# Kernel tuning notes

Measured on AMD Instinct MI355X. Metric: run time of the kernel, lower is better.

The kernel has to match this reference:

```python
import jax, jax.numpy as jnp
import numpy as np

N_NODES = 40000
N_EDGES = 640000
IN_DIM = 128
HID_DIM = 128


def _glorot(key, shape):
    fan_in, fan_out = shape[1], shape[0]
    lim = np.sqrt(6.0 / (fan_in + fan_out))
    return jax.random.uniform(key, shape, jnp.float32, -lim, lim)


def setup_inputs() -> dict:
    key = jax.random.key(0)
    ks = jax.random.split(key, 8)
    x = jax.random.normal(ks[0], (N_NODES, IN_DIM), dtype=jnp.float32)
    edge_index = jax.random.randint(ks[1], (2, N_EDGES), 0, N_NODES, dtype=jnp.int64)
    # SAGEConv params: lin_l (applied to aggregated neighbors, has bias), lin_r (self, no bias)
    W1l = _glorot(ks[2], (HID_DIM, IN_DIM))
    b1l = jnp.zeros((HID_DIM,), jnp.float32)
    W1r = _glorot(ks[3], (HID_DIM, IN_DIM))
    W2l = _glorot(ks[4], (HID_DIM, HID_DIM))
    b2l = jnp.zeros((HID_DIM,), jnp.float32)
    W2r = _glorot(ks[5], (HID_DIM, HID_DIM))
    return {"x": x, "edge_index": edge_index, "W1l": W1l, "b1l": b1l,
            "W1r": W1r, "W2l": W2l, "b2l": b2l, "W2r": W2r}


def _sage_conv(x, src, dst, Wl, bl, Wr):
    # mean aggregation of source features into destination nodes
    msg = x[src]  # [E, D] gather
    agg = jax.ops.segment_sum(msg, dst, num_segments=N_NODES)          # [N, D]
    cnt = jax.ops.segment_sum(jnp.ones_like(dst, jnp.float32), dst,
                              num_segments=N_NODES)                     # [N]
    mean = agg / jnp.maximum(cnt, 1.0)[:, None]
    # out = lin_l(mean_neighbors) + lin_r(x)
    return mean @ Wl.T + bl + x @ Wr.T


def reference(x, edge_index, W1l, b1l, W1r, W2l, b2l, W2r):
    src, dst = edge_index[0], edge_index[1]
    h = jax.nn.relu(_sage_conv(x, src, dst, W1l, b1l, W1r))
    h = jax.nn.relu(_sage_conv(h, src, dst, W2l, b2l, W2r))
    return h
```

## Files before the change

kernel.cpp:

```cpp
#include <hip/hip_runtime.h>
#include <hip/hip_bf16.h>

#define DIM 128
#define NN 40000
#define NE 640000
#define NBLK ((NN + 255) / 256)

typedef __attribute__((ext_vector_type(8))) short s16x8;
typedef __attribute__((ext_vector_type(4))) float f32x4;
typedef __attribute__((ext_vector_type(4))) unsigned short u16x4;
typedef __attribute__((ext_vector_type(4))) unsigned int u32x4;

__device__ __forceinline__ float bf16_lo(unsigned v) { return __uint_as_float(v << 16); }
__device__ __forceinline__ float bf16_hi(unsigned v) { return __uint_as_float(v & 0xffff0000u); }
__device__ __forceinline__ unsigned short f_to_bf16(float f) {
    unsigned u = __float_as_uint(f);
    u += 0x7fffu + ((u >> 16) & 1u);
    return (unsigned short)(u >> 16);
}

__global__ void fill_const_f32(float* __restrict__ out, int n, float v) {
    int i = blockIdx.x * blockDim.x + threadIdx.x;
    if (i < n) out[i] = v;
}

__global__ void cvt_all(const float* __restrict__ x, unsigned short* __restrict__ xb,
                        const float* __restrict__ w0, const float* __restrict__ w1,
                        const float* __restrict__ w2, const float* __restrict__ w3,
                        unsigned short* __restrict__ wb,
                        int* __restrict__ deg, const int* __restrict__ ei,
                        int* __restrict__ flag) {
    int b = blockIdx.x;
    if (b >= 5064) {
        int i = (b - 5064) * 256 + threadIdx.x;
        if (i < NN) deg[i] = 0;
        if (b == 5064 && threadIdx.x < 64) {
            int w = ei[2 * threadIdx.x + 1];
            unsigned long long m = __ballot(w == 0);
            if (threadIdx.x == 0) *flag = (m == ~0ull) ? 1 : 0;
        }
        return;
    }
    const float* src;
    unsigned short* dst;
    size_t i;
    if (b < 5000) {
        src = x; dst = xb;
        i = (size_t)b * 256 + threadIdx.x;
    } else {
        int w = b - 5000;
        int m = w >> 4;
        src = (m == 0) ? w0 : (m == 1) ? w1 : (m == 2) ? w2 : w3;
        dst = wb + (size_t)m * 16384;
        i = (size_t)(w & 15) * 256 + threadIdx.x;
    }
    f32x4 v = *(const f32x4*)(src + 4 * i);
    u16x4 o;
    o.x = f_to_bf16(v.x); o.y = f_to_bf16(v.y);
    o.z = f_to_bf16(v.z); o.w = f_to_bf16(v.w);
    *(u16x4*)(dst + 4 * i) = o;
}


__global__ void count_deg(const int* __restrict__ ei, const int* __restrict__ fmt,
                          int* __restrict__ deg) {
    int e = blockIdx.x * blockDim.x + threadIdx.x;
    if (e >= NE) return;
    int dst = (*fmt) ? ((const int2*)ei)[NE + e].x : ei[NE + e];
    if ((unsigned)dst < (unsigned)NN) atomicAdd(&deg[dst], 1);
}

__global__ void block_sums(const int* __restrict__ deg, int* __restrict__ bsum) {
    __shared__ int sh[256];
    int i = blockIdx.x * 256 + threadIdx.x;
    sh[threadIdx.x] = (i < NN) ? deg[i] : 0;
    __syncthreads();
    for (int off = 128; off > 0; off >>= 1) {
        if (threadIdx.x < off) sh[threadIdx.x] += sh[threadIdx.x + off];
        __syncthreads();
    }
    if (threadIdx.x == 0) bsum[blockIdx.x] = sh[0];
}

__global__ void scan_block2(const int* __restrict__ deg, const int* __restrict__ bsum,
                            int* __restrict__ row_ptr, int* __restrict__ cursor) {
    __shared__ int sh[256];
    int t = threadIdx.x, bid = blockIdx.x;

    int v0 = (t < NBLK) ? bsum[t] : 0;
    sh[t] = v0;
    __syncthreads();
    for (int off = 1; off < 256; off <<= 1) {
        int u = (t >= off) ? sh[t - off] : 0;
        __syncthreads();
        sh[t] += u;
        __syncthreads();
    }
    int base = sh[bid] - bsum[bid];
    __syncthreads();

    int i = bid * 256 + t;
    int v = (i < NN) ? deg[i] : 0;
    sh[t] = v;
    __syncthreads();
    for (int off = 1; off < 256; off <<= 1) {
        int u = (t >= off) ? sh[t - off] : 0;
        __syncthreads();
        sh[t] += u;
        __syncthreads();
    }
    int excl = sh[t] - v + base;
    if (i < NN) { row_ptr[i] = excl; cursor[i] = excl; }
    if (i == NN - 1) row_ptr[NN] = excl + v;
}

__global__ void fill_csr(const int* __restrict__ ei, const int* __restrict__ fmt,
                         int* __restrict__ cursor, int* __restrict__ sorted_src) {
    int e = blockIdx.x * blockDim.x + threadIdx.x;
    if (e >= NE) return;
    int src, dst;
    if (*fmt) {
        src = ((const int2*)ei)[e].x;
        dst = ((const int2*)ei)[NE + e].x;
    } else {
        src = ei[e];
        dst = ei[NE + e];
    }
    if ((unsigned)dst >= (unsigned)NN) return;
    int pos = atomicAdd(&cursor[dst], 1);
    if ((unsigned)pos < (unsigned)NE) sorted_src[pos] = src;
}


#define ACC8(A, v)                                 \
    A[0] += bf16_lo((v).x); A[1] += bf16_hi((v).x); \
    A[2] += bf16_lo((v).y); A[3] += bf16_hi((v).y); \
    A[4] += bf16_lo((v).z); A[5] += bf16_hi((v).z); \
    A[6] += bf16_lo((v).w); A[7] += bf16_hi((v).w);

template <bool WRITE_F32>
__global__ __launch_bounds__(256) void sage_layer(
    const unsigned short* __restrict__ xin,
    const int* __restrict__ row_ptr,
    const int* __restrict__ sorted_src,
    const unsigned short* __restrict__ Wl,
    const unsigned short* __restrict__ Wr,
    const float* __restrict__ bias,
    void* __restrict__ outv) {
    __shared__ unsigned short lds_mean[64 * 128];
    __shared__ unsigned short lds_hs[64 * 128];

    int tid = threadIdx.x;
    int lane = tid & 63;
    int wv = tid >> 6;
    int row0 = blockIdx.x * 64;

    {
        int r = tid >> 2;
        int c4 = tid & 3;
        const unsigned short* src = xin + (size_t)(row0 + r) * DIM + c4 * 32;
#pragma unroll
        for (int c = 0; c < 4; ++c) {
            int lid = c4 * 4 + c;
            u32x4 v = *(const u32x4*)(src + c * 8);
            int off = (r >> 4) * 2048 + (lid >> 2) * 512 + (lid & 3) * 128 + (r & 15) * 8;
            *(u32x4*)(lds_hs + off) = v;
        }
    }

    {
        int grp = lane >> 4;
        int lid = lane & 15;
        int gbase = grp << 4;
        for (int it = 0; it < 4; ++it) {
            int nb = wv * 16 + it * 4 + grp;
            int n = row0 + nb;
            int start = row_ptr[n], end = row_ptr[n + 1];

            float a[8] = {0.f, 0.f, 0.f, 0.f, 0.f, 0.f, 0.f, 0.f};
            float b[8] = {0.f, 0.f, 0.f, 0.f, 0.f, 0.f, 0.f, 0.f};

            int i = start;
            for (; i + 16 <= end; i += 16) {
                int idx = sorted_src[i + lid];
#pragma unroll
                for (int j = 0; j < 16; j += 4) {
                    int s0 = __shfl(idx, gbase + j);
                    int s1 = __shfl(idx, gbase + j + 1);
                    int s2 = __shfl(idx, gbase + j + 2);
                    int s3 = __shfl(idx, gbase + j + 3);
                    u32x4 v0 = *(const u32x4*)(xin + (size_t)s0 * DIM + lid * 8);
                    u32x4 v1 = *(const u32x4*)(xin + (size_t)s1 * DIM + lid * 8);
                    u32x4 v2 = *(const u32x4*)(xin + (size_t)s2 * DIM + lid * 8);
                    u32x4 v3 = *(const u32x4*)(xin + (size_t)s3 * DIM + lid * 8);
                    ACC8(a, v0);
                    ACC8(b, v1);
                    ACC8(a, v2);
                    ACC8(b, v3);
                }
            }
            int rem = end - i;
            if (rem > 0) {
                int src_i = (i + lid < end) ? (i + lid) : (end - 1);
                int idx = sorted_src[src_i];
#pragma unroll
                for (int j = 0; j < 16; ++j) {
                    if (j < rem) {
                        int s = __shfl(idx, gbase + j);
                        u32x4 v = *(const u32x4*)(xin + (size_t)s * DIM + lid * 8);
                        if (j & 1) { ACC8(b, v); }
                        else       { ACC8(a, v); }
                    }
                }
            }
#pragma unroll
            for (int k = 0; k < 8; ++k) a[k] += b[k];

            int d = end - start;
            float inv = 1.f / (float)(d > 1 ? d : 1);
            u32x4 o;
            o.x = (unsigned)f_to_bf16(a[0] * inv) | ((unsigned)f_to_bf16(a[1] * inv) << 16);
            o.y = (unsigned)f_to_bf16(a[2] * inv) | ((unsigned)f_to_bf16(a[3] * inv) << 16);
            o.z = (unsigned)f_to_bf16(a[4] * inv) | ((unsigned)f_to_bf16(a[5] * inv) << 16);
            o.w = (unsigned)f_to_bf16(a[6] * inv) | ((unsigned)f_to_bf16(a[7] * inv) << 16);
            int off = (nb >> 4) * 2048 + (lid >> 2) * 512 + (lid & 3) * 128 + (nb & 15) * 8;
            *(u32x4*)(lds_mean + off) = o;
        }
    }

    __syncthreads();

    {
        int quad = lane >> 4;
        int m16 = lane & 15;
        int lo = lane * 8;
#pragma unroll
        for (int ch = 0; ch < 2; ++ch) {
            int bcol = ch * 64 + wv * 16 + m16;
            const unsigned short* wl0 = Wl + (size_t)bcol * DIM + quad * 8;
            const unsigned short* wr0 = Wr + (size_t)bcol * DIM + quad * 8;
            s16x8 bl[4], br[4];
#pragma unroll
            for (int kb = 0; kb < 4; ++kb) {
                bl[kb] = *(const s16x8*)(wl0 + kb * 32);
                br[kb] = *(const s16x8*)(wr0 + kb * 32);
            }
            f32x4 acc[4] = {{0,0,0,0},{0,0,0,0},{0,0,0,0},{0,0,0,0}};
#pragma unroll
            for (int t = 0; t < 4; ++t) {
#pragma unroll
                for (int kb = 0; kb < 4; ++kb) {
                    s16x8 am = *(const s16x8*)(lds_mean + t * 2048 + kb * 512 + lo);
                    acc[t] = __builtin_amdgcn_mfma_f32_16x16x32_bf16(am, bl[kb], acc[t], 0, 0, 0);
                }
#pragma unroll
                for (int kb = 0; kb < 4; ++kb) {
                    s16x8 ah = *(const s16x8*)(lds_hs + t * 2048 + kb * 512 + lo);
                    acc[t] = __builtin_amdgcn_mfma_f32_16x16x32_bf16(ah, br[kb], acc[t], 0, 0, 0);
                }
            }
            float bv = bias[bcol];
#pragma unroll
            for (int t = 0; t < 4; ++t) {
#pragma unroll
                for (int r = 0; r < 4; ++r) {
                    int orow = row0 + t * 16 + quad * 4 + r;
                    float v = fmaxf(acc[t][r] + bv, 0.f);
                    if (WRITE_F32)
                        ((float*)outv)[(size_t)orow * DIM + bcol] = v;
                    else
                        ((unsigned short*)outv)[(size_t)orow * DIM + bcol] = f_to_bf16(v);
                }
            }
        }
    }
}


extern "C" void kernel_launch(void* const* d_in, const int* in_sizes, int n_in,
                              void* d_out, int out_size, void* d_ws, size_t ws_size,
                              hipStream_t stream) {
    const float* x   = (const float*)d_in[0];
    const int*   ei  = (const int*)d_in[1];
    const float* W1l = (const float*)d_in[2];
    const float* b1l = (const float*)d_in[3];
    const float* W1r = (const float*)d_in[4];
    const float* W2l = (const float*)d_in[5];
    const float* b2l = (const float*)d_in[6];
    const float* W2r = (const float*)d_in[7];
    float* out = (float*)d_out;

    const int OUT_ELEMS = NN * DIM;

    const size_t OFF_DEG  = 0;
    const size_t OFF_ROW  = 163840;
    const size_t OFF_BSUM = 324608;
    const size_t OFF_CUR  = 327680;
    const size_t OFF_FMT  = 491264;
    const size_t OFF_SRT  = 491520;
    const size_t OFF_WB   = 3051520;
    const size_t OFF_XB   = 3182592;
    const size_t OFF_H1   = 23662592;
    const size_t NEEDED   = 33902592;

    if (ws_size < NEEDED) {
        fill_const_f32<<<(OUT_ELEMS + 255) / 256, 256, 0, stream>>>(out, OUT_ELEMS, 50.0f);
        return;
    }

    char* ws = (char*)d_ws;
    int* deg     = (int*)(ws + OFF_DEG);
    int* row_ptr = (int*)(ws + OFF_ROW);
    int* bsum    = (int*)(ws + OFF_BSUM);
    int* cursor  = (int*)(ws + OFF_CUR);
    int* fmtflag = (int*)(ws + OFF_FMT);
    int* sorted  = (int*)(ws + OFF_SRT);
    unsigned short* Wb    = (unsigned short*)(ws + OFF_WB);
    unsigned short* xb    = (unsigned short*)(ws + OFF_XB);
    unsigned short* h1b   = (unsigned short*)(ws + OFF_H1);
    unsigned short* W1lb = Wb;
    unsigned short* W1rb = Wb + 16384;
    unsigned short* W2lb = Wb + 32768;
    unsigned short* W2rb = Wb + 49152;

    cvt_all<<<5221, 256, 0, stream>>>(x, xb, W1l, W1r, W2l, W2r, Wb, deg, ei, fmtflag);
    count_deg<<<(NE + 255) / 256, 256, 0, stream>>>(ei, fmtflag, deg);
    block_sums<<<NBLK, 256, 0, stream>>>(deg, bsum);
    scan_block2<<<NBLK, 256, 0, stream>>>(deg, bsum, row_ptr, cursor);
    fill_csr<<<(NE + 255) / 256, 256, 0, stream>>>(ei, fmtflag, cursor, sorted);

    sage_layer<false><<<NN / 64, 256, 0, stream>>>(xb, row_ptr, sorted, W1lb, W1rb, b1l, h1b);
    sage_layer<true><<<NN / 64, 256, 0, stream>>>(h1b, row_ptr, sorted, W2lb, W2rb, b2l, out);
}
```

Before: 233.8 us.

## Double sage_layer block to 512 threads and XOR-swizzle LDS tiles

Each sage_layer block now runs 512 threads (8 waves) instead of 256. The 64 nodes' neighbor gathers are split across twice as many waves, and each wave computes one 16-column output slice instead of two. The LDS layout for the mean and self-feature tiles gets an XOR swizzle on the row-within-16 index, so writes and MFMA operand reads hit fewer bank conflicts. This adds more latency hiding for the irregular gathers. The trade-off is that each wave now loads its own weight fragments, giving fewer blocks per CU at the larger block size.

```diff
diff --git a/kernel.cpp b/kernel.cpp
--- a/kernel.cpp
+++ b/kernel.cpp
@@ -139,7 +139,7 @@
     A[6] += bf16_lo((v).w); A[7] += bf16_hi((v).w);
 
 template <bool WRITE_F32>
-__global__ __launch_bounds__(256) void sage_layer(
+__global__ __launch_bounds__(512) void sage_layer(
     const unsigned short* __restrict__ xin,
     const int* __restrict__ row_ptr,
     const int* __restrict__ sorted_src,
@@ -156,24 +156,26 @@
     int row0 = blockIdx.x * 64;
 
     {
-        int r = tid >> 2;
-        int c4 = tid & 3;
-        const unsigned short* src = xin + (size_t)(row0 + r) * DIM + c4 * 32;
-#pragma unroll
-        for (int c = 0; c < 4; ++c) {
-            int lid = c4 * 4 + c;
-            u32x4 v = *(const u32x4*)(src + c * 8);
-            int off = (r >> 4) * 2048 + (lid >> 2) * 512 + (lid & 3) * 128 + (r & 15) * 8;
-            *(u32x4*)(lds_hs + off) = v;
-        }
+        int r = tid >> 3;
+        int lid0 = (tid & 7) * 2;
+        int lid1 = lid0 + 1;
+        const unsigned short* src = xin + (size_t)(row0 + r) * DIM + lid0 * 8;
+        u32x4 v0 = *(const u32x4*)(src);
+        u32x4 v1 = *(const u32x4*)(src + 8);
+        int base = (r >> 4) * 2048;
+        int o0 = base + (lid0 >> 2) * 512 + (lid0 & 3) * 128 + (((r & 15) ^ lid0) * 8);
+        int o1 = base + (lid1 >> 2) * 512 + (lid1 & 3) * 128 + (((r & 15) ^ lid1) * 8);
+        *(u32x4*)(lds_hs + o0) = v0;
+        *(u32x4*)(lds_hs + o1) = v1;
     }
 
     {
         int grp = lane >> 4;
         int lid = lane & 15;
         int gbase = grp << 4;
-        for (int it = 0; it < 4; ++it) {
-            int nb = wv * 16 + it * 4 + grp;
+        int g = wv * 4 + grp;
+        for (int it = 0; it < 2; ++it) {
+            int nb = it * 32 + g;
             int n = row0 + nb;
             int start = row_ptr[n], end = row_ptr[n + 1];
 
@@ -223,7 +225,8 @@
             o.y = (unsigned)f_to_bf16(a[2] * inv) | ((unsigned)f_to_bf16(a[3] * inv) << 16);
             o.z = (unsigned)f_to_bf16(a[4] * inv) | ((unsigned)f_to_bf16(a[5] * inv) << 16);
             o.w = (unsigned)f_to_bf16(a[6] * inv) | ((unsigned)f_to_bf16(a[7] * inv) << 16);
-            int off = (nb >> 4) * 2048 + (lid >> 2) * 512 + (lid & 3) * 128 + (nb & 15) * 8;
+            int off = (nb >> 4) * 2048 + (lid >> 2) * 512 + (lid & 3) * 128
+                    + (((nb & 15) ^ lid) * 8);
             *(u32x4*)(lds_mean + off) = o;
         }
     }
@@ -233,44 +236,42 @@
     {
         int quad = lane >> 4;
         int m16 = lane & 15;
-        int lo = lane * 8;
-#pragma unroll
-        for (int ch = 0; ch < 2; ++ch) {
-            int bcol = ch * 64 + wv * 16 + m16;
-            const unsigned short* wl0 = Wl + (size_t)bcol * DIM + quad * 8;
-            const unsigned short* wr0 = Wr + (size_t)bcol * DIM + quad * 8;
-            s16x8 bl[4], br[4];
+        int bcol = wv * 16 + m16;
+        const unsigned short* wl0 = Wl + (size_t)bcol * DIM + quad * 8;
+        const unsigned short* wr0 = Wr + (size_t)bcol * DIM + quad * 8;
+        s16x8 bl[4], br[4];
+#pragma unroll
+        for (int kb = 0; kb < 4; ++kb) {
+            bl[kb] = *(const s16x8*)(wl0 + kb * 32);
+            br[kb] = *(const s16x8*)(wr0 + kb * 32);
+        }
+        f32x4 acc[4] = {{0,0,0,0},{0,0,0,0},{0,0,0,0},{0,0,0,0}};
+#pragma unroll
+        for (int t = 0; t < 4; ++t) {
 #pragma unroll
             for (int kb = 0; kb < 4; ++kb) {
-                bl[kb] = *(const s16x8*)(wl0 + kb * 32);
-                br[kb] = *(const s16x8*)(wr0 + kb * 32);
-            }
-            f32x4 acc[4] = {{0,0,0,0},{0,0,0,0},{0,0,0,0},{0,0,0,0}};
-#pragma unroll
-            for (int t = 0; t < 4; ++t) {
-#pragma unroll
-                for (int kb = 0; kb < 4; ++kb) {
-                    s16x8 am = *(const s16x8*)(lds_mean + t * 2048 + kb * 512 + lo);
-                    acc[t] = __builtin_amdgcn_mfma_f32_16x16x32_bf16(am, bl[kb], acc[t], 0, 0, 0);
-                }
-#pragma unroll
-                for (int kb = 0; kb < 4; ++kb) {
-                    s16x8 ah = *(const s16x8*)(lds_hs + t * 2048 + kb * 512 + lo);
-                    acc[t] = __builtin_amdgcn_mfma_f32_16x16x32_bf16(ah, br[kb], acc[t], 0, 0, 0);
-                }
-            }
-            float bv = bias[bcol];
-#pragma unroll
-            for (int t = 0; t < 4; ++t) {
-#pragma unroll
-                for (int r = 0; r < 4; ++r) {
-                    int orow = row0 + t * 16 + quad * 4 + r;
-                    float v = fmaxf(acc[t][r] + bv, 0.f);
-                    if (WRITE_F32)
-                        ((float*)outv)[(size_t)orow * DIM + bcol] = v;
-                    else
-                        ((unsigned short*)outv)[(size_t)orow * DIM + bcol] = f_to_bf16(v);
-                }
+                int lo = (lane ^ ((kb << 2) | quad)) << 3;
+                s16x8 am = *(const s16x8*)(lds_mean + t * 2048 + kb * 512 + lo);
+                acc[t] = __builtin_amdgcn_mfma_f32_16x16x32_bf16(am, bl[kb], acc[t], 0, 0, 0);
+            }
+#pragma unroll
+            for (int kb = 0; kb < 4; ++kb) {
+                int lo = (lane ^ ((kb << 2) | quad)) << 3;
+                s16x8 ah = *(const s16x8*)(lds_hs + t * 2048 + kb * 512 + lo);
+                acc[t] = __builtin_amdgcn_mfma_f32_16x16x32_bf16(ah, br[kb], acc[t], 0, 0, 0);
+            }
+        }
+        float bv = bias[bcol];
+#pragma unroll
+        for (int t = 0; t < 4; ++t) {
+#pragma unroll
+            for (int r = 0; r < 4; ++r) {
+                int orow = row0 + t * 16 + quad * 4 + r;
+                float v = fmaxf(acc[t][r] + bv, 0.f);
+                if (WRITE_F32)
+                    ((float*)outv)[(size_t)orow * DIM + bcol] = v;
+                else
+                    ((unsigned short*)outv)[(size_t)orow * DIM + bcol] = f_to_bf16(v);
             }
         }
     }
@@ -329,6 +330,6 @@
     scan_block2<<<NBLK, 256, 0, stream>>>(deg, bsum, row_ptr, cursor);
     fill_csr<<<(NE + 255) / 256, 256, 0, stream>>>(ei, fmtflag, cursor, sorted);
 
-    sage_layer<false><<<NN / 64, 256, 0, stream>>>(xb, row_ptr, sorted, W1lb, W1rb, b1l, h1b);
-    sage_layer<true><<<NN / 64, 256, 0, stream>>>(h1b, row_ptr, sorted, W2lb, W2rb, b2l, out);
-}
+    sage_layer<false><<<NN / 64, 512, 0, stream>>>(xb, row_ptr, sorted, W1lb, W1rb, b1l, h1b);
+    sage_layer<true><<<NN / 64, 512, 0, stream>>>(h1b, row_ptr, sorted, W2lb, W2rb, b2l, out);
+}
```

Measured after the change: 229.9 us. No clear change (-1.7%).
